# Kernel optimization log

Measured on AMD Instinct MI355X. Metric: run time of the kernel, lower is better.

The kernel has to match this reference:

```python
import jax, jax.numpy as jnp
import numpy as np

# Forward-arg scalars from the original torch signature (mixed-kappa branch):
KAPPA = 0.5          # 0 < kappa < 1 -> exercises C, V, grad, corr_loss, whit_loss
# compute_grad=True, compute_loss=True, batched=False


def setup_inputs() -> dict:
    key = jax.random.key(0)
    x = jax.random.normal(key, (8, 4096, 1024), dtype=jnp.float32)  # (b, l, d)
    return {"x": x}


def reference(x):
    # batched=False: flatten (b, l, d) -> (M, d)
    b, l, d = x.shape
    xf = x.reshape(b * l, d)                      # (M, d)
    M = xf.shape[0]

    # mean outer product over samples: (1/M) * X^T X, instead of
    # materializing the huge (M, d, d) broadcast tensor the torch code builds.
    mean_outer = jnp.einsum('mi,mj->ij', xf, xf) / M   # (d, d)
    eye = jnp.eye(d, dtype=x.dtype)
    mean_C = mean_outer * (1.0 - eye)             # diagonal zeroed (mean of C)
    mean_V = jnp.mean(xf * xf, axis=0) - 1.0      # (d,) mean of diag(C) - 1

    # grad = mean over M of [(1-kappa)*C  with  diag += kappa*V]
    grad = (1.0 - KAPPA) * mean_C + KAPPA * jnp.diag(mean_V)

    # corr_loss = mean over (M, d, d) of C*C with zeroed diagonal:
    #   sum_{i!=j} (x_i x_j)^2 = (sum_i x_i^2)^2 - sum_i x_i^4 per sample
    sq = xf * xf                                  # (M, d)
    sum_sq = jnp.sum(sq, axis=-1)                 # (M,)
    sum_quart = jnp.sum(sq * sq, axis=-1)         # (M,)
    corr_loss = jnp.mean(sum_sq * sum_sq - sum_quart) / (d * d)

    # whit_loss = mean((x^2 - 1)^2)
    whit_loss = jnp.mean((sq - 1.0) ** 2)

    return grad, corr_loss, whit_loss
```

## Files before the change

### kernel.cpp

```cpp
#include <hip/hip_runtime.h>
#include <hip/hip_bf16.h>
#include <stdint.h>
#include <stddef.h>


#define D_DIM 1024
#define M_ROWS 32768
#define BK 128
#define NKBS (M_ROWS / BK)
#define NT2 10
#define CPT_U32 32768
#define CT_STRIDE 2097152

typedef __attribute__((ext_vector_type(4))) float f32x4;
typedef __attribute__((ext_vector_type(4))) int i32x4;
typedef __attribute__((ext_vector_type(8))) int i32x8;

__device__ inline unsigned short f2bf(float f) {
  unsigned int b = __float_as_uint(f);
  return (unsigned short)((b + 0x7fffu + ((b >> 16) & 1u)) >> 16);
}

__device__ inline void gload_lds16(const void* g, void* l) {
  __builtin_amdgcn_global_load_lds(
      (const __attribute__((address_space(1))) void*)g,
      (__attribute__((address_space(3))) void*)l,
      16, 0, 0);
}

__device__ inline float dppsum16(float v) {
  v += __uint_as_float((unsigned)__builtin_amdgcn_update_dpp(
      0, (int)__float_as_uint(v), 0xB1, 0xF, 0xF, true));
  v += __uint_as_float((unsigned)__builtin_amdgcn_update_dpp(
      0, (int)__float_as_uint(v), 0x4E, 0xF, 0xF, true));
  v += __uint_as_float((unsigned)__builtin_amdgcn_update_dpp(
      0, (int)__float_as_uint(v), 0x141, 0xF, 0xF, true));
  v += __uint_as_float((unsigned)__builtin_amdgcn_update_dpp(
      0, (int)__float_as_uint(v), 0x140, 0xF, 0xF, true));
  return v;
}

__global__ __launch_bounds__(256) void k_pass1(const float* __restrict__ x,
                                               unsigned char* __restrict__ xt,
                                               float* __restrict__ rssp,
                                               float* __restrict__ rs4p) {
  __shared__ unsigned int sh32[16 * 68];
  const int bid = blockIdx.x;
  const int mt = bid & 511;
  const int m0 = mt * 64;
  const int ct = bid >> 9;
  const int c0 = ct * 64;
  const int t = (int)threadIdx.x;
  const int q = t >> 4;
  const int cg = t & 15;

  unsigned int p[4];
  float ss[4], s4[4];
#pragma unroll
  for (int mi = 0; mi < 4; ++mi) {
    const float4 v = *(const float4*)(x + (size_t)(m0 + q * 4 + mi) * D_DIM + c0 + cg * 4);
    const float q0 = v.x * v.x, q1 = v.y * v.y, q2 = v.z * v.z, q3 = v.w * v.w;
    ss[mi] = q0 + q1 + q2 + q3;
    s4[mi] = q0 * q0 + q1 * q1 + q2 * q2 + q3 * q3;
    unsigned int u = (unsigned int)__builtin_amdgcn_cvt_pk_fp8_f32(v.x, v.y, 0, false);
    p[mi] = (unsigned int)__builtin_amdgcn_cvt_pk_fp8_f32(v.z, v.w, (int)u, true);
  }
#pragma unroll
  for (int mi = 0; mi < 4; ++mi) {
    ss[mi] = dppsum16(ss[mi]);
    s4[mi] = dppsum16(s4[mi]);
  }
  if (cg == 0) {
#pragma unroll
    for (int mi = 0; mi < 4; ++mi) {
      rssp[ct * M_ROWS + m0 + q * 4 + mi] = ss[mi];
      rs4p[ct * M_ROWS + m0 + q * 4 + mi] = s4[mi];
    }
  }

  const unsigned int t01l = __builtin_amdgcn_perm(p[1], p[0], 0x05010400u);
  const unsigned int t01h = __builtin_amdgcn_perm(p[1], p[0], 0x07030602u);
  const unsigned int t23l = __builtin_amdgcn_perm(p[3], p[2], 0x05010400u);
  const unsigned int t23h = __builtin_amdgcn_perm(p[3], p[2], 0x07030602u);
  uint4 w;
  w.x = __builtin_amdgcn_perm(t23l, t01l, 0x05040100u);
  w.y = __builtin_amdgcn_perm(t23l, t01l, 0x07060302u);
  w.z = __builtin_amdgcn_perm(t23h, t01h, 0x05040100u);
  w.w = __builtin_amdgcn_perm(t23h, t01h, 0x07060302u);
  *(uint4*)&sh32[q * 68 + cg * 4] = w;
  __syncthreads();

  const int c = t >> 2, mh = t & 3;
  uint4 o;
  o.x = sh32[(mh * 4 + 0) * 68 + c];
  o.y = sh32[(mh * 4 + 1) * 68 + c];
  o.z = sh32[(mh * 4 + 2) * 68 + c];
  o.w = sh32[(mh * 4 + 3) * 68 + c];
  *(uint4*)(xt + (size_t)ct * CT_STRIDE + ((size_t)mt << 12) + t * 16) = o;
}

__global__ __launch_bounds__(512, 2) void k_gemm(const unsigned char* __restrict__ xt,
                                                 unsigned int* __restrict__ cpart,
                                                 int S, int swz) {
  __shared__ unsigned char As[2][32768];
  __shared__ unsigned char Bs[2][32768];
  const int bid = (int)blockIdx.x;
  int s, tidx;
  if (swz) {
    const int xcd = bid & 7;
    tidx = (bid >> 3) % NT2;
    s = (bid / (8 * NT2)) * 8 + xcd;
  } else {
    s = bid / NT2;
    tidx = bid - s * NT2;
  }
  int rem = tidx, ti = 0;
  while (rem >= 4 - ti) { rem -= 4 - ti; ++ti; }
  const int tj = ti + rem;

  const int t = (int)threadIdx.x;
  const int l = t & 63, w = t >> 6;
  const int wr2 = w >> 2, wc4 = w & 3;
  const int r = l & 15, g = l >> 4;

  f32x4 acc[8][4];
#pragma unroll
  for (int mi = 0; mi < 8; ++mi)
#pragma unroll
    for (int ni = 0; ni < 4; ++ni) acc[mi][ni] = (f32x4){0.f, 0.f, 0.f, 0.f};

  const int srow = t >> 3;
  const int slot = (t & 7) ^ (srow & 7);
  const int slterm = (slot >> 2) * 4096 + (slot & 3) * 16;
  const unsigned char* pa[4];
  const unsigned char* pb[4];
#pragma unroll
  for (int j = 0; j < 4; ++j) {
    pa[j] = xt + (size_t)(ti * 4 + j) * CT_STRIDE + srow * 64 + slterm;
    pb[j] = xt + (size_t)(tj * 4 + j) * CT_STRIDE + srow * 64 + slterm;
  }

#define STAGE(B, K) do { \
    const size_t koff = (size_t)(K) << 6; \
    _Pragma("unroll") \
    for (int j = 0; j < 4; ++j) { \
      gload_lds16(pa[j] + koff, &As[B][j * 8192 + t * 16]); \
      gload_lds16(pb[j] + koff, &Bs[B][j * 8192 + t * 16]); \
    } \
  } while (0)

  const int swb = r & 7;
  const int oA0 = (((2 * g + 0) ^ swb) << 4);
  const int oA1 = (((2 * g + 1) ^ swb) << 4);
  const int arow = (wr2 * 128 + r) * 128;
  const int brow = (wc4 * 64 + r) * 128;

  const int kq = NKBS / S, kr = NKBS - kq * S;
  const int kb0 = s * kq + (s < kr ? s : kr);
  const int nkb = kq + (s < kr ? 1 : 0);
  int kb = kb0 * BK;

  STAGE(0, kb);
  STAGE(1, kb + BK);

  for (int it = 0; it < nkb; ++it) {
    if (it == nkb - 1)
      asm volatile("s_waitcnt vmcnt(0)" ::: "memory");
    else
      asm volatile("s_waitcnt vmcnt(8)" ::: "memory");
    __builtin_amdgcn_s_barrier();

    const unsigned char* Ab = As[it & 1];
    const unsigned char* Bb = Bs[it & 1];
    i32x8 a8[8], b8[4];
#pragma unroll
    for (int mi = 0; mi < 8; ++mi) {
      const i32x4 lo = *(const i32x4*)(Ab + arow + mi * 2048 + oA0);
      const i32x4 hi = *(const i32x4*)(Ab + arow + mi * 2048 + oA1);
      a8[mi] = (i32x8){lo[0], lo[1], lo[2], lo[3], hi[0], hi[1], hi[2], hi[3]};
    }
#pragma unroll
    for (int ni = 0; ni < 4; ++ni) {
      const i32x4 lo = *(const i32x4*)(Bb + brow + ni * 2048 + oA0);
      const i32x4 hi = *(const i32x4*)(Bb + brow + ni * 2048 + oA1);
      b8[ni] = (i32x8){lo[0], lo[1], lo[2], lo[3], hi[0], hi[1], hi[2], hi[3]};
    }
    asm volatile("s_waitcnt lgkmcnt(0)" ::: "memory");
    __builtin_amdgcn_s_barrier();

    if (it + 2 < nkb) STAGE(it & 1, kb + 2 * BK);

    __builtin_amdgcn_s_setprio(1);
#pragma unroll
    for (int ni = 0; ni < 4; ++ni)
#pragma unroll
      for (int mi = 0; mi < 8; ++mi)
        acc[mi][ni] = __builtin_amdgcn_mfma_scale_f32_16x16x128_f8f6f4(
            a8[mi], b8[ni], acc[mi][ni], 0, 0, 0, 0x7F7F7F7Fu, 0, 0x7F7F7F7Fu);
    __builtin_amdgcn_s_setprio(0);
    kb += BK;
  }
#undef STAGE

  unsigned int* cp = cpart + ((size_t)s * NT2 + tidx) * CPT_U32;
#pragma unroll
  for (int mi = 0; mi < 8; ++mi) {
    const int rowb = wr2 * 128 + mi * 16 + g * 4;
#pragma unroll
    for (int ni = 0; ni < 4; ++ni) {
      const int col = wc4 * 64 + ni * 16 + r;
      const unsigned int w0 = (unsigned int)f2bf(acc[mi][ni][0]) |
                              ((unsigned int)f2bf(acc[mi][ni][1]) << 16);
      const unsigned int w1 = (unsigned int)f2bf(acc[mi][ni][2]) |
                              ((unsigned int)f2bf(acc[mi][ni][3]) << 16);
      cp[(size_t)((rowb >> 1) + 0) * 256 + col] = w0;
      cp[(size_t)((rowb >> 1) + 1) * 256 + col] = w1;
    }
  }
}

__global__ __launch_bounds__(256) void k_epi(const unsigned int* __restrict__ cpart,
                                             float* __restrict__ out, int S) {
  __shared__ float smir[8][260];
  const int b = (int)blockIdx.x;
  const int tile = b >> 5, chunk = b & 31;
  int rem = tile, ti = 0;
  while (rem >= 4 - ti) { rem -= 4 - ti; ++ti; }
  const int tj = ti + rem;
  const int t = (int)threadIdx.x;
  const int qq = (chunk * 256 + t) * 4;
  const int rpl = t >> 6;
  const int c = (t & 63) * 4;

  const unsigned int* cp = cpart + (size_t)tile * CPT_U32 + qq;
  const size_t st = (size_t)NT2 * CPT_U32;
  float lo0 = 0.f, lo1 = 0.f, lo2 = 0.f, lo3 = 0.f;
  float hi0 = 0.f, hi1 = 0.f, hi2 = 0.f, hi3 = 0.f;
  for (int s = 0; s < S; ++s) {
    const uint4 v = *(const uint4*)(cp + (size_t)s * st);
    lo0 += __uint_as_float(v.x << 16); hi0 += __uint_as_float(v.x & 0xFFFF0000u);
    lo1 += __uint_as_float(v.y << 16); hi1 += __uint_as_float(v.y & 0xFFFF0000u);
    lo2 += __uint_as_float(v.z << 16); hi2 += __uint_as_float(v.z & 0xFFFF0000u);
    lo3 += __uint_as_float(v.w << 16); hi3 += __uint_as_float(v.w & 0xFFFF0000u);
  }

  const float sc = 0.5f / (float)M_ROWS;
  f32x4 lo = (f32x4){lo0 * sc, lo1 * sc, lo2 * sc, lo3 * sc};
  f32x4 hi = (f32x4){hi0 * sc, hi1 * sc, hi2 * sc, hi3 * sc};

  const int gi = ti * 256 + chunk * 8 + 2 * rpl;
  const int gj = tj * 256 + c;
  if (ti == tj) {
#pragma unroll
    for (int kk = 0; kk < 4; ++kk) {
      if (gi == gj + kk) lo[kk] -= 0.5f;
      if (gi + 1 == gj + kk) hi[kk] -= 0.5f;
    }
  }
  *(f32x4*)(out + (size_t)gi * D_DIM + gj) = lo;
  *(f32x4*)(out + (size_t)(gi + 1) * D_DIM + gj) = hi;

  if (ti != tj) {
    const int jr = 2 * rpl;
    *(f32x4*)&smir[jr][c] = lo;
    *(f32x4*)&smir[jr + 1][c] = hi;
    __syncthreads();
    const int cc = t;
    f32x4 m0v, m1v;
    m0v[0] = smir[0][cc]; m0v[1] = smir[1][cc];
    m0v[2] = smir[2][cc]; m0v[3] = smir[3][cc];
    m1v[0] = smir[4][cc]; m1v[1] = smir[5][cc];
    m1v[2] = smir[6][cc]; m1v[3] = smir[7][cc];
    float* ob = out + (size_t)(tj * 256 + cc) * D_DIM + ti * 256 + chunk * 8;
    *(f32x4*)(ob + 0) = m0v;
    *(f32x4*)(ob + 4) = m1v;
  }
}

__global__ __launch_bounds__(256) void k_fin1(const float* __restrict__ rssp,
                                              const float* __restrict__ rs4p,
                                              float* __restrict__ scp) {
  __shared__ float sm[3][4];
  const int t = (int)threadIdx.x;
  const int m = (int)blockIdx.x * 256 + t;
  float a = 0.f, b = 0.f;
#pragma unroll
  for (int ct = 0; ct < 16; ++ct) {
    a += rssp[ct * M_ROWS + m];
    b += rs4p[ct * M_ROWS + m];
  }
  float corr = a * a - b;
#pragma unroll
  for (int off = 32; off; off >>= 1) {
    corr += __shfl_down(corr, off);
    a += __shfl_down(a, off);
    b += __shfl_down(b, off);
  }
  const int wv = t >> 6;
  if ((t & 63) == 0) { sm[0][wv] = corr; sm[1][wv] = a; sm[2][wv] = b; }
  __syncthreads();
  if (t == 0) {
    float c4 = 0.f, a4 = 0.f, b4 = 0.f;
#pragma unroll
    for (int i = 0; i < 4; ++i) { c4 += sm[0][i]; a4 += sm[1][i]; b4 += sm[2][i]; }
    scp[(int)blockIdx.x * 4 + 0] = c4;
    scp[(int)blockIdx.x * 4 + 1] = a4;
    scp[(int)blockIdx.x * 4 + 2] = b4;
  }
}

__global__ __launch_bounds__(128) void k_fin2(const float* __restrict__ scp,
                                              float* __restrict__ out) {
  __shared__ float sm[3][2];
  const int t = (int)threadIdx.x;
  float c = scp[t * 4 + 0], a = scp[t * 4 + 1], b = scp[t * 4 + 2];
#pragma unroll
  for (int off = 32; off; off >>= 1) {
    c += __shfl_down(c, off);
    a += __shfl_down(a, off);
    b += __shfl_down(b, off);
  }
  const int wv = t >> 6;
  if ((t & 63) == 0) { sm[0][wv] = c; sm[1][wv] = a; sm[2][wv] = b; }
  __syncthreads();
  if (t == 0) {
    const double ct = (double)sm[0][0] + (double)sm[0][1];
    const double st = (double)sm[1][0] + (double)sm[1][1];
    const double qt = (double)sm[2][0] + (double)sm[2][1];
    const double N = (double)M_ROWS * (double)D_DIM;
    out[1048576] = (float)(ct / (double)M_ROWS / ((double)D_DIM * (double)D_DIM));
    out[1048577] = (float)((qt - 2.0 * st + N) / N);
  }
}

extern "C" void kernel_launch(void* const* d_in, const int* in_sizes, int n_in,
                              void* d_out, int out_size, void* d_ws, size_t ws_size,
                              hipStream_t stream) {
  (void)in_sizes; (void)n_in; (void)out_size;
  const float* x = (const float*)d_in[0];
  float* out = (float*)d_out;
  char* ws = (char*)d_ws;

  unsigned char* xt = (unsigned char*)ws;
  float* rssp = (float*)(ws + 33554432);
  float* rs4p = (float*)(ws + 35651584);
  float* scp  = (float*)(ws + 37748736);
  unsigned int* cpart = (unsigned int*)(ws + 37752832);
  const size_t base = 37752832;
  size_t avail = (ws_size > base) ? (ws_size - base) : 0;
  int S = (int)(avail / (sizeof(unsigned int) * NT2 * CPT_U32));
  if (S > 24) S = 24;
  int swz = 0;
  if (S >= 8) { S &= ~7; swz = 1; }
  if (S < 1) S = 1;

  k_pass1<<<8192, 256, 0, stream>>>(x, xt, rssp, rs4p);
  k_gemm<<<NT2 * S, 512, 0, stream>>>(xt, cpart, S, swz);
  k_epi<<<NT2 * 32, 256, 0, stream>>>(cpart, out, S);
  k_fin1<<<128, 256, 0, stream>>>(rssp, rs4p, scp);
  k_fin2<<<1, 128, 0, stream>>>(scp, out);
}
```

Before: 75.84 us.

## Split MFMA k-step into four phases interleaving LDS reads with matrix ops

Result: no change. 77.21 us (+1.8%).

```diff
diff --git a/kernel.cpp b/kernel.cpp
--- a/kernel.cpp
+++ b/kernel.cpp
@@ -155,6 +155,25 @@
   const int arow = (wr2 * 128 + r) * 128;
   const int brow = (wc4 * 64 + r) * 128;
 
+#define RD_A(mi) do { \
+    const i32x4 lo_ = *(const i32x4*)(Ab + arow + (mi) * 2048 + oA0); \
+    const i32x4 hi_ = *(const i32x4*)(Ab + arow + (mi) * 2048 + oA1); \
+    a8[mi] = (i32x8){lo_[0], lo_[1], lo_[2], lo_[3], hi_[0], hi_[1], hi_[2], hi_[3]}; \
+  } while (0)
+#define RD_B(ni) do { \
+    const i32x4 lo_ = *(const i32x4*)(Bb + brow + (ni) * 2048 + oA0); \
+    const i32x4 hi_ = *(const i32x4*)(Bb + brow + (ni) * 2048 + oA1); \
+    b8[ni] = (i32x8){lo_[0], lo_[1], lo_[2], lo_[3], hi_[0], hi_[1], hi_[2], hi_[3]}; \
+  } while (0)
+#define MM(mi, ni) \
+    acc[mi][ni] = __builtin_amdgcn_mfma_scale_f32_16x16x128_f8f6f4( \
+        a8[mi], b8[ni], acc[mi][ni], 0, 0, 0, 0x7F7F7F7Fu, 0, 0x7F7F7F7Fu)
+#define PH_SYNC() do { \
+    __builtin_amdgcn_s_barrier(); \
+    asm volatile("s_waitcnt lgkmcnt(0)" ::: "memory"); \
+    __builtin_amdgcn_sched_barrier(0); \
+  } while (0)
+
   const int kq = NKBS / S, kr = NKBS - kq * S;
   const int kb0 = s * kq + (s < kr ? s : kr);
   const int nkb = kq + (s < kr ? 1 : 0);
@@ -173,34 +192,43 @@
     const unsigned char* Ab = As[it & 1];
     const unsigned char* Bb = Bs[it & 1];
     i32x8 a8[8], b8[4];
-#pragma unroll
-    for (int mi = 0; mi < 8; ++mi) {
-      const i32x4 lo = *(const i32x4*)(Ab + arow + mi * 2048 + oA0);
-      const i32x4 hi = *(const i32x4*)(Ab + arow + mi * 2048 + oA1);
-      a8[mi] = (i32x8){lo[0], lo[1], lo[2], lo[3], hi[0], hi[1], hi[2], hi[3]};
-    }
-#pragma unroll
-    for (int ni = 0; ni < 4; ++ni) {
-      const i32x4 lo = *(const i32x4*)(Bb + brow + ni * 2048 + oA0);
-      const i32x4 hi = *(const i32x4*)(Bb + brow + ni * 2048 + oA1);
-      b8[ni] = (i32x8){lo[0], lo[1], lo[2], lo[3], hi[0], hi[1], hi[2], hi[3]};
-    }
-    asm volatile("s_waitcnt lgkmcnt(0)" ::: "memory");
+
+    RD_B(0); RD_B(1); RD_A(0); RD_A(1); RD_A(2); RD_A(3);
+    PH_SYNC();
+    __builtin_amdgcn_s_setprio(1);
+    MM(0, 0); MM(0, 1); MM(1, 0); MM(1, 1);
+    MM(2, 0); MM(2, 1); MM(3, 0); MM(3, 1);
+    __builtin_amdgcn_s_setprio(0);
     __builtin_amdgcn_s_barrier();
 
+    RD_A(4); RD_A(5); RD_A(6); RD_A(7);
+    PH_SYNC();
+    __builtin_amdgcn_s_setprio(1);
+    MM(4, 0); MM(4, 1); MM(5, 0); MM(5, 1);
+    MM(6, 0); MM(6, 1); MM(7, 0); MM(7, 1);
+    __builtin_amdgcn_s_setprio(0);
+    __builtin_amdgcn_s_barrier();
+
+    RD_B(2); RD_B(3);
+    PH_SYNC();
+    __builtin_amdgcn_s_setprio(1);
+    MM(0, 2); MM(0, 3); MM(1, 2); MM(1, 3);
+    MM(2, 2); MM(2, 3); MM(3, 2); MM(3, 3);
+    __builtin_amdgcn_s_setprio(0);
+    __builtin_amdgcn_s_barrier();
+
     if (it + 2 < nkb) STAGE(it & 1, kb + 2 * BK);
-
     __builtin_amdgcn_s_setprio(1);
-#pragma unroll
-    for (int ni = 0; ni < 4; ++ni)
-#pragma unroll
-      for (int mi = 0; mi < 8; ++mi)
-        acc[mi][ni] = __builtin_amdgcn_mfma_scale_f32_16x16x128_f8f6f4(
-            a8[mi], b8[ni], acc[mi][ni], 0, 0, 0, 0x7F7F7F7Fu, 0, 0x7F7F7F7Fu);
+    MM(4, 2); MM(4, 3); MM(5, 2); MM(5, 3);
+    MM(6, 2); MM(6, 3); MM(7, 2); MM(7, 3);
     __builtin_amdgcn_s_setprio(0);
     kb += BK;
   }
 #undef STAGE
+#undef RD_A
+#undef RD_B
+#undef MM
+#undef PH_SYNC
 
   unsigned int* cp = cpart + ((size_t)s * NT2 + tidx) * CPT_U32;
 #pragma unroll
```
